# Performance work log

Measured on AMD Instinct MI355X. Metric: run time of the kernel, lower is better.

## Reference

```python
import jax, jax.numpy as jnp
import numpy as np

LEAK = 0.01  # F.leaky_relu default negative_slope
TAU = 1.0    # sinkhorn_tau
ITERS = 5    # sinkhorn_iters


def leaky_relu(x):
    return jnp.where(x >= 0, x, LEAK * x)


def setup_inputs() -> dict:
    key = jax.random.key(0)
    B, N, F, E, H, L = 512, 200, 32, 128, 128, 2
    ks = jax.random.split(key, 8)
    def s(k, shape, fan_in):
        return jax.random.normal(k, shape, dtype=jnp.float32) * (1.0 / np.sqrt(fan_in)).astype(np.float32)
    return {
        "x": jax.random.normal(ks[0], (B, N, F), dtype=jnp.float32),
        "w_emb": s(ks[1], (E, F), F),
        "b_emb": jnp.zeros((E,), jnp.float32),
        "w_ih": s(ks[2], (L, 4 * H, E), H),   # stacked per-layer LSTM input weights
        "w_hh": s(ks[3], (L, 4 * H, H), H),   # stacked per-layer LSTM recurrent weights
        "b_ih": jnp.zeros((L, 4 * H), jnp.float32),
        "b_hh": jnp.zeros((L, 4 * H), jnp.float32),
        "w_fc1": s(ks[4], (E, H), H),
        "b_fc1": jnp.zeros((E,), jnp.float32),
        "w_fc2": s(ks[5], (N, E), E),
        "b_fc2": jnp.zeros((N,), jnp.float32),
        "do_round": 0,  # non-differentiable Hungarian rounding path disabled
    }


def _lstm_layer(xs, h0, c0, Wih, Whh, b):
    # xs: [N, B, E]  (seq-major, like torch.nn.LSTM); h0, c0: [B, H]
    def step(carry, x_t):
        h, c = carry
        g = x_t @ Wih.T + h @ Whh.T + b               # [B, 4H]
        i, f, gg, o = jnp.split(g, 4, axis=-1)        # torch gate order i,f,g,o
        c = jax.nn.sigmoid(f) * c + jax.nn.sigmoid(i) * jnp.tanh(gg)
        h = jax.nn.sigmoid(o) * jnp.tanh(c)
        return (h, c), h
    (hN, cN), hs = jax.lax.scan(step, (h0, c0), xs)
    return hs, hN, cN


def _sinkhorn(M, tau, n_iters):
    # exp(M / tau) followed by alternating row / column normalization
    x = jnp.exp(M / tau)
    for _ in range(n_iters):
        x = x / jnp.sum(x, axis=2, keepdims=True)  # row normalize
        x = x / jnp.sum(x, axis=1, keepdims=True)  # column normalize
    return x


def reference(x, w_emb, b_emb, w_ih, w_hh, b_ih, b_hh, w_fc1, b_fc1, w_fc2, b_fc2, do_round):
    # do_round=0: the Hungarian rounding branch (host round-trip) is skipped;
    # the module then returns just the Sinkhorn output psi.
    B = x.shape[0]
    H = w_hh.shape[-1]
    e = leaky_relu(x @ w_emb.T + b_emb)            # [B, N, E]
    xs = jnp.transpose(e, (1, 0, 2))               # [N, B, E]
    h = jnp.zeros((B, H), x.dtype)
    c = jnp.zeros((B, H), x.dtype)
    hs = xs
    # NB: original code feeds the SAME embedded x to every LSTM layer,
    # carrying only the (h, c) state between layers.
    for l in range(w_ih.shape[0]):
        hs, h, c = _lstm_layer(xs, h, c, w_ih[l], w_hh[l], b_ih[l] + b_hh[l])
    out = jnp.transpose(hs, (1, 0, 2))             # [B, N, H]
    out = leaky_relu(out @ w_fc1.T + b_fc1)        # [B, N, E]
    M = out @ w_fc2.T + b_fc2                      # [B, N, N]
    psi = _sinkhorn(M, TAU, ITERS)
    return psi
```

## Files before the change

### kernel.cpp

```cpp
#include <hip/hip_runtime.h>
#include <cstdint>
#include <cstddef>

#define LEAK 0.01f
#define L2E 1.4426950408889634f

typedef _Float16 f16;
typedef __attribute__((ext_vector_type(4))) _Float16 f16x4;
typedef __attribute__((ext_vector_type(8))) _Float16 f16x8;
typedef __attribute__((ext_vector_type(4))) float f32x4;

static __device__ __forceinline__ f16x8 pack8s(float4 a, float4 b, float s) {
  f16x8 r;
  r[0] = (f16)(a.x * s); r[1] = (f16)(a.y * s); r[2] = (f16)(a.z * s); r[3] = (f16)(a.w * s);
  r[4] = (f16)(b.x * s); r[5] = (f16)(b.y * s); r[6] = (f16)(b.z * s); r[7] = (f16)(b.w * s);
  return r;
}
static __device__ __forceinline__ f16x8 pack8(float4 a, float4 b) {
  return pack8s(a, b, 1.0f);
}
#define MFMA16(a, b, c) __builtin_amdgcn_mfma_f32_16x16x32_f16((a), (b), (c), 0, 0, 0)

__constant__ float SCG[4] = {L2E, L2E, 2.0f * L2E, L2E};

__global__ __launch_bounds__(256) void k_emb(
    const float* __restrict__ x, const float* __restrict__ wemb,
    const float* __restrict__ bemb, f16* __restrict__ e) {
  const int t = blockIdx.x, tid = threadIdx.x;
  __shared__ __align__(16) float wl[128 * 32];
  __shared__ float bl[128];
  for (int idx = tid; idx < 1024; idx += 256)
    ((float4*)wl)[idx] = ((const float4*)wemb)[idx];
  if (tid < 128) bl[tid] = bemb[tid];

  float xa[32], xb[32];
  const float* xpa = x + ((size_t)tid * 200 + t) * 32;
  const float* xpb = x + ((size_t)(tid + 256) * 200 + t) * 32;
#pragma unroll
  for (int k4 = 0; k4 < 8; ++k4) {
    float4 va = *(const float4*)(xpa + k4 * 4);
    float4 vb = *(const float4*)(xpb + k4 * 4);
    xa[k4 * 4 + 0] = va.x; xa[k4 * 4 + 1] = va.y; xa[k4 * 4 + 2] = va.z; xa[k4 * 4 + 3] = va.w;
    xb[k4 * 4 + 0] = vb.x; xb[k4 * 4 + 1] = vb.y; xb[k4 * 4 + 2] = vb.z; xb[k4 * 4 + 3] = vb.w;
  }
  __syncthreads();

  f16* ea = e + ((size_t)t * 512 + tid) * 128;
  f16* eb = e + ((size_t)t * 512 + tid + 256) * 128;
  for (int j8 = 0; j8 < 16; ++j8) {
    f16x8 oa, ob;
#pragma unroll
    for (int jj = 0; jj < 8; ++jj) {
      int j = j8 * 8 + jj;
      float aa = bl[j], ab = bl[j];
#pragma unroll
      for (int k4 = 0; k4 < 8; ++k4) {
        float4 wv = *(const float4*)&wl[j * 32 + k4 * 4];
        aa += xa[k4 * 4 + 0] * wv.x + xa[k4 * 4 + 1] * wv.y +
              xa[k4 * 4 + 2] * wv.z + xa[k4 * 4 + 3] * wv.w;
        ab += xb[k4 * 4 + 0] * wv.x + xb[k4 * 4 + 1] * wv.y +
              xb[k4 * 4 + 2] * wv.z + xb[k4 * 4 + 3] * wv.w;
      }
      oa[jj] = (f16)(aa >= 0.f ? aa : LEAK * aa);
      ob[jj] = (f16)(ab >= 0.f ? ab : LEAK * ab);
    }
    *(f16x8*)(ea + j8 * 8) = oa;
    *(f16x8*)(eb + j8 * 8) = ob;
  }
}

static __device__ __forceinline__ void xp_waves(
    const f16* __restrict__ e, const float* __restrict__ wih,
    const float* __restrict__ bih, const float* __restrict__ bhh,
    f16* __restrict__ xp, int t0, int wid, int nrep, int stride, int lane) {
  const int q = lane >> 4, l16 = lane & 15;
  const int ct = wid & 7;

  f16x8 BW[4][4];
  float bias[4];
#pragma unroll
  for (int G = 0; G < 4; ++G) {
    int n = G * 128 + ct * 16 + l16;
    bias[G] = (bih[n] + bhh[n]) * SCG[G];
#pragma unroll
    for (int kc = 0; kc < 4; ++kc) {
      const float4* p = (const float4*)(wih + (size_t)n * 128 + kc * 32 + q * 8);
      BW[G][kc] = pack8s(p[0], p[1], SCG[G]);
    }
  }
  for (int rep = 0; rep < nrep; ++rep) {
    int task = wid + rep * stride;
    int g2 = task >> 3;
    int tl = g2 >> 2, btg = g2 & 3;
#pragma unroll
    for (int p = 0; p < 8; ++p) {
      int bt = btg * 8 + p;
      const f16* A = e + ((size_t)(t0 + tl) * 512 + bt * 16 + l16) * 128 + q * 8;
      f16x8 af[4];
#pragma unroll
      for (int kc = 0; kc < 4; ++kc) af[kc] = *(const f16x8*)(A + kc * 32);
      f32x4 acc[4];
#pragma unroll
      for (int G = 0; G < 4; ++G)
        acc[G] = (f32x4){bias[G], bias[G], bias[G], bias[G]};
#pragma unroll
      for (int kc = 0; kc < 4; ++kc)
#pragma unroll
        for (int G = 0; G < 4; ++G)
          acc[G] = MFMA16(af[kc], BW[G][kc], acc[G]);
      f16x8 oA, oB;
#pragma unroll
      for (int r = 0; r < 4; ++r) {
        oA[r]     = (f16)acc[0][r];
        oA[4 + r] = (f16)acc[1][r];
        oB[r]     = (f16)acc[2][r];
        oB[4 + r] = (f16)acc[3][r];
      }
      f16* dst = xp + (size_t)tl * 262144 + bt * 8192 + ct * 1024 + lane * 16;
      *(f16x8*)dst = oA;
      *(f16x8*)(dst + 8) = oB;
    }
  }
}

__global__ __launch_bounds__(256, 2) void k_xp(
    const f16* __restrict__ e, const float* __restrict__ wih,
    const float* __restrict__ bih, const float* __restrict__ bhh,
    f16* __restrict__ xp, int t0) {
  xp_waves(e, wih, bih, bhh, xp, t0,
           blockIdx.x * 4 + (threadIdx.x >> 6), 1, 0, threadIdx.x & 63);
}

static __device__ __forceinline__ void rec_body(
    const f16* __restrict__ xp, const float* __restrict__ whh,
    float* __restrict__ hws, float* __restrict__ cws,
    f16* __restrict__ hs, int layer, int t0, int CH, int bt) {
  const int tid = threadIdx.x;
  const int w = tid >> 6, lane = tid & 63, q = lane >> 4, l16 = lane & 15;
  __shared__ __align__(16) f16 hlds[2][16][136];

  f16x8 BH[4][4];
#pragma unroll
  for (int G = 0; G < 4; ++G) {
    int n = G * 128 + w * 16 + l16;
#pragma unroll
    for (int kc = 0; kc < 4; ++kc) {
      const float4* ph = (const float4*)(whh + (size_t)n * 128 + kc * 32 + q * 8);
      BH[G][kc] = pack8s(ph[0], ph[1], SCG[G]);
    }
  }

  f32x4 cst;
  if (layer == 0 && t0 == 0) {
    cst = (f32x4){0.f, 0.f, 0.f, 0.f};
    for (int idx = tid; idx < 2 * 16 * 136; idx += 512)
      ((f16*)hlds)[idx] = (f16)0.f;
  } else {
    cst = *(const f32x4*)(cws + ((size_t)(bt * 8 + w) * 64 + lane) * 4);
    f32x4 hv = *(const f32x4*)(hws + ((size_t)(bt * 8 + w) * 64 + lane) * 4);
#pragma unroll
    for (int r = 0; r < 4; ++r)
      hlds[1][q * 4 + r][w * 16 + l16] = (f16)hv[r];
  }
  __syncthreads();

  const f16* xpl = xp + (((size_t)bt * 8 + w) * 64 + lane) * 16;
  f16x8 xa = *(const f16x8*)(xpl);
  f16x8 xb = *(const f16x8*)(xpl + 8);

  f32x4 hk;
  const int srow = tid >> 5, scol = (tid & 31) * 4;
  for (int tl = 0; tl < CH; ++tl) {
    int tn = (tl + 1 < CH) ? tl + 1 : tl;
    const f16* xpn = xpl + (size_t)tn * 262144;
    f16x8 nxa = *(const f16x8*)(xpn);
    f16x8 nxb = *(const f16x8*)(xpn + 8);

    const int rb = (tl + 1) & 1;
    f16x8 ah[4];
#pragma unroll
    for (int kc = 0; kc < 4; ++kc)
      ah[kc] = *(const f16x8*)&hlds[rb][l16][kc * 32 + q * 8];

    f32x4 acc[4];
#pragma unroll
    for (int r = 0; r < 4; ++r) {
      acc[0][r] = (float)xa[r];
      acc[1][r] = (float)xa[4 + r];
      acc[2][r] = (float)xb[r];
      acc[3][r] = (float)xb[4 + r];
    }
#pragma unroll
    for (int kc = 0; kc < 4; ++kc)
#pragma unroll
      for (int G = 0; G < 4; ++G)
        acc[G] = MFMA16(ah[kc], BH[G][kc], acc[G]);

    const int wb = tl & 1;
#pragma unroll
    for (int r = 0; r < 4; ++r) {
      float ui = __builtin_amdgcn_exp2f(-acc[0][r]);
      float uf = __builtin_amdgcn_exp2f(-acc[1][r]);
      float ug = __builtin_amdgcn_exp2f(-fmaxf(acc[2][r], -88.f));
      float uo = __builtin_amdgcn_exp2f(-acc[3][r]);
      float sf = __builtin_amdgcn_rcpf(1.0f + uf);
      float p1 = (1.0f - ug) * __builtin_amdgcn_rcpf((1.0f + ui) * (1.0f + ug));
      float cc = sf * cst[r] + p1;
      cst[r] = cc;
      float ccl = fminf(fmaxf(cc, -30.f), 30.f) * (-2.0f * L2E);
      float ucc = __builtin_amdgcn_exp2f(ccl);
      float hv = (1.0f - ucc) * __builtin_amdgcn_rcpf((1.0f + uo) * (1.0f + ucc));
      hk[r] = hv;
      hlds[wb][q * 4 + r][w * 16 + l16] = (f16)hv;
    }
    __syncthreads();
    if (layer != 0) {
      f16x4 hv4 = *(const f16x4*)&hlds[wb][srow][scol];
      *(f16x4*)(hs + ((size_t)(bt * 16 + srow) * 200 + (t0 + tl)) * 128 + scol) = hv4;
    }
    xa = nxa; xb = nxb;
  }

  *(f32x4*)(hws + ((size_t)(bt * 8 + w) * 64 + lane) * 4) = hk;
  *(f32x4*)(cws + ((size_t)(bt * 8 + w) * 64 + lane) * 4) = cst;
}

__global__ __launch_bounds__(512, 2) void k_rec(
    const f16* __restrict__ xp, const float* __restrict__ whh,
    float* __restrict__ hws, float* __restrict__ cws,
    f16* __restrict__ hs, int layer, int t0, int CH) {
  rec_body(xp, whh, hws, cws, hs, layer, t0, CH, blockIdx.x);
}

__global__ __launch_bounds__(512, 2) void k_recxp(
    const f16* __restrict__ xp_r, const float* __restrict__ whh,
    float* __restrict__ hws, float* __restrict__ cws,
    f16* __restrict__ hs, int layer, int t0_r,
    const f16* __restrict__ e, const float* __restrict__ wih_n,
    const float* __restrict__ bih_n, const float* __restrict__ bhh_n,
    f16* __restrict__ xp_w, int t0_x) {
  if (blockIdx.x < 32) {
    rec_body(xp_r, whh, hws, cws, hs, layer, t0_r, 100, blockIdx.x);
  } else {
    int wid = (blockIdx.x - 32) * 8 + (threadIdx.x >> 6);
    if (wid < 3200)
      xp_waves(e, wih_n, bih_n, bhh_n, xp_w, t0_x, wid, 1, 0, threadIdx.x & 63);
  }
}

__global__ __launch_bounds__(256, 2) void k_head(
    const f16* __restrict__ hs, const float* __restrict__ wfc1,
    const float* __restrict__ bfc1, const float* __restrict__ wfc2,
    const float* __restrict__ bfc2, float* __restrict__ psi) {
  extern __shared__ char smem[];
  f16* E = (f16*)smem;
  f16* o1 = (f16*)(smem + 27200);
  float* uu = (float*)(smem + 80000);
  float* vv = (float*)(smem + 80800);
  const int b = blockIdx.x, tid = threadIdx.x;
  const int w = tid >> 6, lane = tid & 63, q = lane >> 4, l16 = lane & 15;
  const f16* A = hs + (size_t)b * 200 * 128;

  f16x8 BF1[2][4];
  float bias1[2];
#pragma unroll
  for (int s = 0; s < 2; ++s) {
    int n = w * 32 + s * 16 + l16;
    bias1[s] = bfc1[n];
#pragma unroll
    for (int kc = 0; kc < 4; ++kc) {
      const float4* p = (const float4*)(wfc1 + (size_t)n * 128 + kc * 32 + q * 8);
      BF1[s][kc] = pack8(p[0], p[1]);
    }
  }
  f16x8 BF2[4][4];
  float bias2[4] = {0.f, 0.f, 0.f, 0.f};
#pragma unroll
  for (int ci = 0; ci < 4; ++ci) {
    int ct = w + ci * 4;
    if (ct < 13) {
      int n = ct * 16 + l16; if (n > 199) n = 199;
      bias2[ci] = bfc2[n];
#pragma unroll
      for (int kc = 0; kc < 4; ++kc) {
        const float4* p = (const float4*)(wfc2 + (size_t)n * 128 + kc * 32 + q * 8);
        BF2[ci][kc] = pack8(p[0], p[1]);
      }
    }
  }

  for (int rt = 0; rt < 13; ++rt) {
    int m = rt * 16 + l16; if (m > 199) m = 199;
    f16x8 af[4];
#pragma unroll
    for (int kc = 0; kc < 4; ++kc)
      af[kc] = *(const f16x8*)(A + (size_t)m * 128 + kc * 32 + q * 8);
#pragma unroll
    for (int s = 0; s < 2; ++s) {
      f32x4 acc = (f32x4){bias1[s], bias1[s], bias1[s], bias1[s]};
#pragma unroll
      for (int kc = 0; kc < 4; ++kc) acc = MFMA16(af[kc], BF1[s][kc], acc);
      int col = w * 32 + s * 16 + l16;
#pragma unroll
      for (int r = 0; r < 4; ++r) {
        int row = rt * 16 + q * 4 + r;
        float vvv = acc[r]; vvv = vvv >= 0.f ? vvv : LEAK * vvv;
        if (row < 200) o1[row * 136 + col] = (f16)vvv;
      }
    }
  }
  __syncthreads();

  for (int rt = 0; rt < 13; ++rt) {
    int m = rt * 16 + l16; if (m > 199) m = 199;
    f16x8 af[4];
#pragma unroll
    for (int kc = 0; kc < 4; ++kc)
      af[kc] = *(const f16x8*)&o1[m * 136 + kc * 32 + q * 8];
    __syncthreads();
#pragma unroll
    for (int ci = 0; ci < 4; ++ci) {
      int ct = w + ci * 4;
      if (ct < 13) {
        f32x4 acc = (f32x4){bias2[ci], bias2[ci], bias2[ci], bias2[ci]};
#pragma unroll
        for (int kc = 0; kc < 4; ++kc) acc = MFMA16(af[kc], BF2[ci][kc], acc);
        int col = ct * 16 + l16;
#pragma unroll
        for (int r = 0; r < 4; ++r) {
          int row = rt * 16 + q * 4 + r;
          if (row < 200 && col < 200) E[row * 200 + col] = (f16)__expf(acc[r]);
        }
      }
    }
  }
  __syncthreads();
  if (tid < 200) vv[tid] = 1.0f;
  __syncthreads();

  for (int it = 0; it < 5; ++it) {
    if (tid < 200) {
      const f16* Er = E + tid * 200;
      float s0 = 0.f, s1 = 0.f;
      for (int j = 0; j < 200; j += 4) {
        f16x4 e4 = *(const f16x4*)(Er + j);
        float4 v4 = *(const float4*)(vv + j);
        s0 += (float)e4[0] * v4.x + (float)e4[1] * v4.y;
        s1 += (float)e4[2] * v4.z + (float)e4[3] * v4.w;
      }
      uu[tid] = __builtin_amdgcn_rcpf(s0 + s1);
    }
    __syncthreads();
    if (tid < 200) {
      float s0 = 0.f, s1 = 0.f;
      for (int i = 0; i < 200; i += 4) {
        float4 u4 = *(const float4*)(uu + i);
        s0 += (float)E[(i + 0) * 200 + tid] * u4.x + (float)E[(i + 1) * 200 + tid] * u4.y;
        s1 += (float)E[(i + 2) * 200 + tid] * u4.z + (float)E[(i + 3) * 200 + tid] * u4.w;
      }
      vv[tid] = __builtin_amdgcn_rcpf(s0 + s1);
    }
    __syncthreads();
  }

  float* P = psi + (size_t)b * 40000;
  for (int idx4 = tid; idx4 < 10000; idx4 += 256) {
    unsigned i = ((unsigned)idx4 * 5243u) >> 18;
    unsigned jq = (unsigned)idx4 - i * 50u;
    f16x4 e4 = *(const f16x4*)(E + i * 200 + jq * 4);
    float4 v4 = *(const float4*)(vv + jq * 4);
    float ui = uu[i];
    float4 o;
    o.x = ui * (float)e4[0] * v4.x;
    o.y = ui * (float)e4[1] * v4.y;
    o.z = ui * (float)e4[2] * v4.z;
    o.w = ui * (float)e4[3] * v4.w;
    *(float4*)(P + i * 200 + jq * 4) = o;
  }
}

extern "C" void kernel_launch(void* const* d_in, const int* in_sizes, int n_in,
                              void* d_out, int out_size, void* d_ws, size_t ws_size,
                              hipStream_t stream) {
  const float* x    = (const float*)d_in[0];
  const float* wemb = (const float*)d_in[1];
  const float* bemb = (const float*)d_in[2];
  const float* wih  = (const float*)d_in[3];
  const float* whh  = (const float*)d_in[4];
  const float* bih  = (const float*)d_in[5];
  const float* bhh  = (const float*)d_in[6];
  const float* wfc1 = (const float*)d_in[7];
  const float* bfc1 = (const float*)d_in[8];
  const float* wfc2 = (const float*)d_in[9];
  const float* bfc2 = (const float*)d_in[10];
  float* psi = (float*)d_out;

  char* ws = (char*)d_ws;
  f16*   e   = (f16*)(ws);
  float* hws = (float*)(ws + 26214400);
  float* cws = (float*)(ws + 26476544);
  f16*   hs  = (f16*)(ws + 26738688);
  f16*   xpA = (f16*)(ws + 52953088);
  f16*   xpB = (f16*)(ws + 105381888);

  const size_t fixed = 52953088;
  const bool pipelined = (ws_size >= 157810688ull);

  (void)hipFuncSetAttribute((const void*)k_head,
                            hipFuncAttributeMaxDynamicSharedMemorySize, 81600);

  k_emb<<<200, 256, 0, stream>>>(x, wemb, bemb, e);

  const float* wih1 = wih + 65536;  const float* whh1 = whh + 65536;
  const float* bih1 = bih + 512;    const float* bhh1 = bhh + 512;

  if (pipelined) {
    k_xp<<<800, 256, 0, stream>>>(e, wih, bih, bhh, xpA, 0);
    k_recxp<<<448, 512, 0, stream>>>(xpA, whh, hws, cws, hs, 0, 0,
                                     e, wih, bih, bhh, xpB, 100);
    k_recxp<<<448, 512, 0, stream>>>(xpB, whh, hws, cws, hs, 0, 100,
                                     e, wih1, bih1, bhh1, xpA, 0);
    k_recxp<<<448, 512, 0, stream>>>(xpA, whh1, hws, cws, hs, 1, 0,
                                     e, wih1, bih1, bhh1, xpB, 100);
    k_rec<<<32, 512, 0, stream>>>(xpB, whh1, hws, cws, hs, 1, 100, 100);
  } else {
    const int cands[] = {100, 50, 40, 25, 20, 10, 8, 5, 4, 2, 1};
    int CH = 1;
    for (int ci = 0; ci < 11; ++ci) {
      if (fixed + (size_t)cands[ci] * 524288 <= ws_size) { CH = cands[ci]; break; }
    }
    for (int l = 0; l < 2; ++l) {
      const float* wih_l = wih + (size_t)l * 65536;
      const float* whh_l = whh + (size_t)l * 65536;
      const float* bih_l = bih + (size_t)l * 512;
      const float* bhh_l = bhh + (size_t)l * 512;
      for (int t0 = 0; t0 < 200; t0 += CH) {
        k_xp<<<CH * 8, 256, 0, stream>>>(e, wih_l, bih_l, bhh_l, xpA, t0);
        k_rec<<<32, 512, 0, stream>>>(xpA, whh_l, hws, cws, hs, l, t0, CH);
      }
    }
  }
  k_head<<<512, 256, 81600, stream>>>(hs, wfc1, bfc1, wfc2, bfc2, psi);
}
```

Baseline: 619.2 us.

## Pack two batch tiles per recurrence block and merge the cell-update reciprocals

Each recurrence block now runs two 16-row batch tiles with 1024 threads and a per-tile LDS buffer. This halves the recurrence block count to 16, and the companion projection blocks are resized to 16 waves each. The cell-state update is rewritten over a common denominator, so one reciprocal replaces two. In exchange, the block-wide barrier now spans 16 waves, and the 1024-thread launch bound with two blocks per CU may squeeze the register budget for the preloaded recurrent weights and cause spills.

```diff
diff --git a/kernel.cpp b/kernel.cpp
--- a/kernel.cpp
+++ b/kernel.cpp
@@ -134,10 +134,13 @@
 static __device__ __forceinline__ void rec_body(
     const f16* __restrict__ xp, const float* __restrict__ whh,
     float* __restrict__ hws, float* __restrict__ cws,
-    f16* __restrict__ hs, int layer, int t0, int CH, int bt) {
+    f16* __restrict__ hs, int layer, int t0, int CH, int bt0) {
   const int tid = threadIdx.x;
-  const int w = tid >> 6, lane = tid & 63, q = lane >> 4, l16 = lane & 15;
-  __shared__ __align__(16) f16 hlds[2][16][136];
+  const int tile = tid >> 9;
+  const int tidl = tid & 511;
+  const int bt = bt0 + tile;
+  const int w = tidl >> 6, lane = tidl & 63, q = lane >> 4, l16 = lane & 15;
+  __shared__ __align__(16) f16 hlds[2][2][16][136];
 
   f16x8 BH[4][4];
 #pragma unroll
@@ -153,14 +156,14 @@
   f32x4 cst;
   if (layer == 0 && t0 == 0) {
     cst = (f32x4){0.f, 0.f, 0.f, 0.f};
-    for (int idx = tid; idx < 2 * 16 * 136; idx += 512)
-      ((f16*)hlds)[idx] = (f16)0.f;
+    for (int idx = tidl; idx < 2 * 16 * 136; idx += 512)
+      ((f16*)hlds[tile])[idx] = (f16)0.f;
   } else {
     cst = *(const f32x4*)(cws + ((size_t)(bt * 8 + w) * 64 + lane) * 4);
     f32x4 hv = *(const f32x4*)(hws + ((size_t)(bt * 8 + w) * 64 + lane) * 4);
 #pragma unroll
     for (int r = 0; r < 4; ++r)
-      hlds[1][q * 4 + r][w * 16 + l16] = (f16)hv[r];
+      hlds[tile][1][q * 4 + r][w * 16 + l16] = (f16)hv[r];
   }
   __syncthreads();
 
@@ -169,7 +172,7 @@
   f16x8 xb = *(const f16x8*)(xpl + 8);
 
   f32x4 hk;
-  const int srow = tid >> 5, scol = (tid & 31) * 4;
+  const int srow = tidl >> 5, scol = (tidl & 31) * 4;
   for (int tl = 0; tl < CH; ++tl) {
     int tn = (tl + 1 < CH) ? tl + 1 : tl;
     const f16* xpn = xpl + (size_t)tn * 262144;
@@ -180,7 +183,7 @@
     f16x8 ah[4];
 #pragma unroll
     for (int kc = 0; kc < 4; ++kc)
-      ah[kc] = *(const f16x8*)&hlds[rb][l16][kc * 32 + q * 8];
+      ah[kc] = *(const f16x8*)&hlds[tile][rb][l16][kc * 32 + q * 8];
 
     f32x4 acc[4];
 #pragma unroll
@@ -203,19 +206,20 @@
       float uf = __builtin_amdgcn_exp2f(-acc[1][r]);
       float ug = __builtin_amdgcn_exp2f(-fmaxf(acc[2][r], -88.f));
       float uo = __builtin_amdgcn_exp2f(-acc[3][r]);
-      float sf = __builtin_amdgcn_rcpf(1.0f + uf);
-      float p1 = (1.0f - ug) * __builtin_amdgcn_rcpf((1.0f + ui) * (1.0f + ug));
-      float cc = sf * cst[r] + p1;
+      float ai = 1.0f + ui, ag = 1.0f + ug, af = 1.0f + uf;
+      float aig = ai * ag;
+      float num = cst[r] * aig + (1.0f - ug) * af;
+      float cc = num * __builtin_amdgcn_rcpf(af * aig);
       cst[r] = cc;
       float ccl = fminf(fmaxf(cc, -30.f), 30.f) * (-2.0f * L2E);
       float ucc = __builtin_amdgcn_exp2f(ccl);
       float hv = (1.0f - ucc) * __builtin_amdgcn_rcpf((1.0f + uo) * (1.0f + ucc));
       hk[r] = hv;
-      hlds[wb][q * 4 + r][w * 16 + l16] = (f16)hv;
+      hlds[tile][wb][q * 4 + r][w * 16 + l16] = (f16)hv;
     }
     __syncthreads();
     if (layer != 0) {
-      f16x4 hv4 = *(const f16x4*)&hlds[wb][srow][scol];
+      f16x4 hv4 = *(const f16x4*)&hlds[tile][wb][srow][scol];
       *(f16x4*)(hs + ((size_t)(bt * 16 + srow) * 200 + (t0 + tl)) * 128 + scol) = hv4;
     }
     xa = nxa; xb = nxb;
@@ -225,24 +229,24 @@
   *(f32x4*)(cws + ((size_t)(bt * 8 + w) * 64 + lane) * 4) = cst;
 }
 
-__global__ __launch_bounds__(512, 2) void k_rec(
+__global__ __launch_bounds__(1024, 2) void k_rec(
     const f16* __restrict__ xp, const float* __restrict__ whh,
     float* __restrict__ hws, float* __restrict__ cws,
     f16* __restrict__ hs, int layer, int t0, int CH) {
-  rec_body(xp, whh, hws, cws, hs, layer, t0, CH, blockIdx.x);
-}
-
-__global__ __launch_bounds__(512, 2) void k_recxp(
+  rec_body(xp, whh, hws, cws, hs, layer, t0, CH, blockIdx.x * 2);
+}
+
+__global__ __launch_bounds__(1024, 2) void k_recxp(
     const f16* __restrict__ xp_r, const float* __restrict__ whh,
     float* __restrict__ hws, float* __restrict__ cws,
     f16* __restrict__ hs, int layer, int t0_r,
     const f16* __restrict__ e, const float* __restrict__ wih_n,
     const float* __restrict__ bih_n, const float* __restrict__ bhh_n,
     f16* __restrict__ xp_w, int t0_x) {
-  if (blockIdx.x < 32) {
-    rec_body(xp_r, whh, hws, cws, hs, layer, t0_r, 100, blockIdx.x);
+  if (blockIdx.x < 16) {
+    rec_body(xp_r, whh, hws, cws, hs, layer, t0_r, 100, blockIdx.x * 2);
   } else {
-    int wid = (blockIdx.x - 32) * 8 + (threadIdx.x >> 6);
+    int wid = (blockIdx.x - 16) * 16 + (threadIdx.x >> 6);
     if (wid < 3200)
       xp_waves(e, wih_n, bih_n, bhh_n, xp_w, t0_x, wid, 1, 0, threadIdx.x & 63);
   }
@@ -416,13 +420,13 @@
 
   if (pipelined) {
     k_xp<<<800, 256, 0, stream>>>(e, wih, bih, bhh, xpA, 0);
-    k_recxp<<<448, 512, 0, stream>>>(xpA, whh, hws, cws, hs, 0, 0,
-                                     e, wih, bih, bhh, xpB, 100);
-    k_recxp<<<448, 512, 0, stream>>>(xpB, whh, hws, cws, hs, 0, 100,
-                                     e, wih1, bih1, bhh1, xpA, 0);
-    k_recxp<<<448, 512, 0, stream>>>(xpA, whh1, hws, cws, hs, 1, 0,
-                                     e, wih1, bih1, bhh1, xpB, 100);
-    k_rec<<<32, 512, 0, stream>>>(xpB, whh1, hws, cws, hs, 1, 100, 100);
+    k_recxp<<<216, 1024, 0, stream>>>(xpA, whh, hws, cws, hs, 0, 0,
+                                      e, wih, bih, bhh, xpB, 100);
+    k_recxp<<<216, 1024, 0, stream>>>(xpB, whh, hws, cws, hs, 0, 100,
+                                      e, wih1, bih1, bhh1, xpA, 0);
+    k_recxp<<<216, 1024, 0, stream>>>(xpA, whh1, hws, cws, hs, 1, 0,
+                                      e, wih1, bih1, bhh1, xpB, 100);
+    k_rec<<<16, 1024, 0, stream>>>(xpB, whh1, hws, cws, hs, 1, 100, 100);
   } else {
     const int cands[] = {100, 50, 40, 25, 20, 10, 8, 5, 4, 2, 1};
     int CH = 1;
@@ -436,7 +440,7 @@
       const float* bhh_l = bhh + (size_t)l * 512;
       for (int t0 = 0; t0 < 200; t0 += CH) {
         k_xp<<<CH * 8, 256, 0, stream>>>(e, wih_l, bih_l, bhh_l, xpA, t0);
-        k_rec<<<32, 512, 0, stream>>>(xpA, whh_l, hws, cws, hs, l, t0, CH);
+        k_rec<<<16, 1024, 0, stream>>>(xpA, whh_l, hws, cws, hs, l, t0, CH);
       }
     }
   }
```

New measurement: 863.6 us. +39.5%, slower.
